# Kernel optimization log

Hardware: AMD Instinct MI355X
Metric: run time of the kernel (lower is better)

Reference implementation:

```python
import jax, jax.numpy as jnp
import numpy as np

B, S, H = 1, 2048, 2048
I = 1408
E = 64
TOP_K = 8
N_GROUP = 8
TOPK_GROUP = 4
SCALE = 2.5
N_SHARED = 2


def setup_inputs() -> dict:
    key = jax.random.key(0)
    ks = jax.random.split(key, 9)
    x = jax.random.normal(ks[0], (B, S, H), dtype=jnp.float32)
    # kaiming_uniform(a=sqrt(5)) for [E, H] weight -> bound = 1/sqrt(H)
    gate_w = jax.random.uniform(ks[1], (E, H), jnp.float32, -1.0, 1.0) / jnp.sqrt(float(H))
    e_bias = jnp.zeros((E,), jnp.float32)
    gate_proj = jax.random.normal(ks[2], (E, I, H), jnp.float32) * 0.02
    up_proj = jax.random.normal(ks[3], (E, I, H), jnp.float32) * 0.02
    down_proj = jax.random.normal(ks[4], (E, H, I), jnp.float32) * 0.02
    SI = I * N_SHARED
    shared_gate_w = jax.random.uniform(ks[5], (SI, H), jnp.float32, -1.0, 1.0) / jnp.sqrt(float(H))
    shared_up_w = jax.random.uniform(ks[6], (SI, H), jnp.float32, -1.0, 1.0) / jnp.sqrt(float(H))
    shared_down_w = jax.random.uniform(ks[7], (H, SI), jnp.float32, -1.0, 1.0) / jnp.sqrt(float(SI))
    return {"hidden_states": x, "gate_w": gate_w, "e_bias": e_bias,
            "gate_proj": gate_proj, "up_proj": up_proj, "down_proj": down_proj,
            "shared_gate_w": shared_gate_w, "shared_up_w": shared_up_w,
            "shared_down_w": shared_down_w}


def _moe_forward(hidden_states, gate_w, e_bias, gate_proj, up_proj, down_proj,
                 shared_gate_w, shared_up_w, shared_down_w):
    bsz, seq_len, h = hidden_states.shape
    xf = hidden_states.reshape(-1, h).astype(jnp.float32)  # [T, H]
    T = bsz * seq_len

    # ---- DeepSeek group-restricted top-k gating ----
    logits = xf @ gate_w.T                                  # [T, E]
    scores = jax.nn.sigmoid(logits)
    scores_for_choice = scores + e_bias[None, :]
    gs = scores_for_choice.reshape(T, N_GROUP, E // N_GROUP)
    group_scores = jax.lax.top_k(gs, 2)[0].sum(-1)          # [T, n_group] sum of top-2 per group
    group_idx = jax.lax.top_k(group_scores, TOPK_GROUP)[1]  # [T, topk_group]
    group_mask = jax.nn.one_hot(group_idx, N_GROUP, dtype=jnp.float32).sum(1)  # [T, n_group]
    score_mask = jnp.repeat(group_mask, E // N_GROUP, axis=1)                  # [T, E]
    tmp_scores = jnp.where(score_mask > 0, scores_for_choice, 0.0)
    topk_idx = jax.lax.top_k(tmp_scores, TOP_K)[1]          # [T, top_k]
    topk_w = jnp.take_along_axis(scores, topk_idx, axis=1)  # gather from UN-biased scores
    topk_w = topk_w / (topk_w.sum(-1, keepdims=True) + 1e-20)
    topk_w = topk_w * SCALE

    # Dense combine weights [T, E]; exactly equivalent to sort/dispatch/combine.
    rows = jnp.arange(T)
    cw = jnp.zeros((T, E), jnp.float32).at[rows[:, None], topk_idx].add(topk_w)

    # ---- per-expert FFN, accumulated with lax.scan over the (fixed) expert axis ----
    def step(y, we):
        Wg, Wu, Wd, w = we                                  # [I,H],[I,H],[H,I],[T]
        g = xf @ Wg.T                                       # [T, I]
        u = xf @ Wu.T
        inter = jax.nn.silu(g) * u                          # silu_mul kernel
        out = inter @ Wd.T                                  # [T, H]
        return y + out * w[:, None], None

    y0 = jnp.zeros_like(xf)
    y, _ = jax.lax.scan(step, y0, (gate_proj, up_proj, down_proj, cw.T))
    y = y.reshape(bsz, seq_len, h)

    # ---- shared experts ----
    sg = hidden_states @ shared_gate_w.T                    # [B, S, SI]
    su = hidden_states @ shared_up_w.T
    shared_out = (jax.nn.silu(sg) * su) @ shared_down_w.T   # [B, S, H]
    return y + shared_out


def reference(hidden_states, gate_w, e_bias, gate_proj, up_proj, down_proj,
              shared_gate_w, shared_up_w, shared_down_w):
    return _moe_forward(hidden_states, gate_w, e_bias, gate_proj, up_proj, down_proj,
                        shared_gate_w, shared_up_w, shared_down_w)
```

## Files before the change

kernel.cpp:

```cpp
#include <hip/hip_runtime.h>

typedef unsigned short u16;
typedef unsigned int u32;
typedef __attribute__((ext_vector_type(8))) short short8;
typedef __attribute__((ext_vector_type(8))) u16 ushort8;
typedef __attribute__((ext_vector_type(4))) float f32x4;

#define T_TOK 2048
#define H_DIM 2048
#define NEXP 64
#define I_DIM 1408
#define SI_DIM 2816
#define BM 128
#define BK 64
#define MAXT 384

__device__ __forceinline__ u16 f2bf(float f) {
    u32 u = __builtin_bit_cast(u32, f);
    u32 r = u + 0x7FFFu + ((u >> 16) & 1u);
    return (u16)(r >> 16);
}

__device__ __forceinline__ ushort8 cvt8(f32x4 a, f32x4 b) {
    ushort8 o;
    o[0] = f2bf(a[0]); o[1] = f2bf(a[1]); o[2] = f2bf(a[2]); o[3] = f2bf(a[3]);
    o[4] = f2bf(b[0]); o[5] = f2bf(b[1]); o[6] = f2bf(b[2]); o[7] = f2bf(b[3]);
    return o;
}

__device__ __forceinline__ f32x4 mfma16(short8 a, short8 b, f32x4 c) {
    return __builtin_amdgcn_mfma_f32_16x16x32_bf16(a, b, c, 0, 0, 0);
}

__global__ __launch_bounds__(256) void k_cvt(const float* __restrict__ x, u16* __restrict__ xb) {
    int i = (blockIdx.x * 256 + threadIdx.x) * 8;
    f32x4 v0 = *(const f32x4*)(x + i);
    f32x4 v1 = *(const f32x4*)(x + i + 4);
    *(ushort8*)(xb + i) = cvt8(v0, v1);
}

__global__ __launch_bounds__(256) void k_gate_logits(const float* __restrict__ x,
        const float* __restrict__ gw, float* __restrict__ logits) {
    __shared__ float xs[8][65];
    __shared__ float wsh[64][65];
    int tid = threadIdx.x;
    int t0 = blockIdx.x * 8;
    double acc0 = 0.0, acc1 = 0.0;
    int e = tid & 63, tg = tid >> 6;
    for (int k0 = 0; k0 < H_DIM; k0 += 64) {
        #pragma unroll
        for (int s = 0; s < 2; ++s) {
            int idx = s * 256 + tid;
            int r = idx >> 6, k = idx & 63;
            xs[r][k] = x[(size_t)(t0 + r) * H_DIM + k0 + k];
        }
        #pragma unroll
        for (int s = 0; s < 16; ++s) {
            int idx = s * 256 + tid;
            int r = idx >> 6, k = idx & 63;
            wsh[r][k] = gw[(size_t)r * H_DIM + k0 + k];
        }
        __syncthreads();
        #pragma unroll 8
        for (int k = 0; k < 64; ++k) {
            double wv = (double)wsh[e][k];
            acc0 += (double)xs[tg][k] * wv;
            acc1 += (double)xs[tg + 4][k] * wv;
        }
        __syncthreads();
    }
    logits[(size_t)(t0 + tg) * NEXP + e] = (float)acc0;
    logits[(size_t)(t0 + tg + 4) * NEXP + e] = (float)acc1;
}

__global__ __launch_bounds__(256) void k_topk(const float* __restrict__ logits,
        const float* __restrict__ ebias, int* __restrict__ topk_idx,
        float* __restrict__ topk_w, int* __restrict__ counts) {
    __shared__ float bsh[64];
    if (threadIdx.x < 64) bsh[threadIdx.x] = ebias[threadIdx.x];
    __syncthreads();
    int t = blockIdx.x * 256 + threadIdx.x;
    float sc[64];
    #pragma unroll
    for (int e2 = 0; e2 < 64; ++e2) {
        float lg = logits[(size_t)t * 64 + e2];
        sc[e2] = 1.0f / (1.0f + expf(-lg));
    }
    float gsc[8];
    #pragma unroll
    for (int g = 0; g < 8; ++g) {
        float m1 = -1e30f, m2 = -1e30f;
        #pragma unroll
        for (int j = 0; j < 8; ++j) {
            float v = sc[g * 8 + j] + bsh[g * 8 + j];
            if (v > m1) { m2 = m1; m1 = v; }
            else if (v > m2) { m2 = v; }
        }
        gsc[g] = m1 + m2;
    }
    u32 gmask = 0;
    #pragma unroll
    for (int it = 0; it < 4; ++it) {
        float best = -1e30f; int bi = 0;
        #pragma unroll
        for (int g = 0; g < 8; ++g) {
            bool ok = !((gmask >> g) & 1u);
            if (ok && gsc[g] > best) { best = gsc[g]; bi = g; }
        }
        gmask |= 1u << bi;
    }
    unsigned long long avail = 0ull;
    #pragma unroll
    for (int g = 0; g < 8; ++g)
        if ((gmask >> g) & 1u) avail |= (0xFFull << (g * 8));
    float wsum = 0.f;
    int idx[8]; float wv[8];
    #pragma unroll
    for (int it = 0; it < 8; ++it) {
        float best = -1e30f, bw = 0.f; int bi = 0;
        #pragma unroll
        for (int e2 = 0; e2 < 64; ++e2) {
            bool ok = (avail >> e2) & 1ull;
            float v = sc[e2] + bsh[e2];
            if (ok && v > best) { best = v; bi = e2; bw = sc[e2]; }
        }
        avail &= ~(1ull << bi);
        idx[it] = bi; wv[it] = bw; wsum += bw;
    }
    float scale = 2.5f / (wsum + 1e-20f);
    #pragma unroll
    for (int it = 0; it < 8; ++it) {
        topk_idx[t * 8 + it] = idx[it];
        topk_w[t * 8 + it] = wv[it] * scale;
        atomicAdd(&counts[idx[it]], 1);
    }
}

__global__ void k_prefix(const int* __restrict__ counts, int* __restrict__ offsets,
                         int* __restrict__ tiles, int* __restrict__ ntiles) {
    if (threadIdx.x == 0) {
        int run = 0;
        for (int e = 0; e < 64; ++e) { offsets[e] = run; run += counts[e]; }
        offsets[64] = run;
        for (int i = 0; i < MAXT; ++i) tiles[i] = -1;
        int slot[8] = {0, 0, 0, 0, 0, 0, 0, 0};
        int nt = 0;
        for (int e = 0; e < 64; ++e) {
            int xcd = e & 7;
            int c = counts[e];
            for (int m0 = 0; m0 < c; m0 += BM) {
                int pos = xcd + 8 * slot[xcd];
                if (pos < MAXT) { tiles[pos] = (e << 16) | m0; slot[xcd]++; nt++; }
            }
        }
        *ntiles = nt;
    }
}

__global__ __launch_bounds__(256) void k_scatter(const int* __restrict__ topk_idx,
        const float* __restrict__ topk_w, const int* __restrict__ offsets,
        int* __restrict__ fill, int* __restrict__ tok_list, float* __restrict__ w_list) {
    int gid = blockIdx.x * 256 + threadIdx.x;
    int t = gid >> 3;
    int e = topk_idx[gid];
    int pos = offsets[e] + atomicAdd(&fill[e], 1);
    tok_list[pos] = t;
    w_list[pos] = topk_w[gid];
}

__global__ __launch_bounds__(256, 2) void k_gateup(
        const u16* __restrict__ xb,
        const float* __restrict__ gate_base, const float* __restrict__ up_base,
        const int* __restrict__ offsets, const int* __restrict__ tok_list,
        const int* __restrict__ tiles, const int* __restrict__ ntiles,
        u16* __restrict__ inter, int Irows) {
    int e, m0, seg, n, i0;
    if (tiles) {
        int tt = tiles[blockIdx.x];
        if (tt < 0) return;
        e = tt >> 16; m0 = tt & 0xFFFF;
        seg = offsets[e]; n = offsets[e + 1] - seg;
        i0 = blockIdx.y * 64;
    } else {
        e = 0; seg = 0; n = T_TOK;
        i0 = blockIdx.x * 64;
        if (i0 >= Irows) return;
        m0 = blockIdx.y * BM;
    }
    if (n <= 0 || m0 >= n) return;

    const float* Bg = gate_base + (size_t)e * Irows * H_DIM;
    const float* Bu = up_base + (size_t)e * Irows * H_DIM;

    __shared__ u16 As[2][BM * BK];
    __shared__ u16 Bsg[2][64 * BK];
    __shared__ u16 Bsu[2][64 * BK];

    int tid = threadIdx.x;
    int w = tid >> 6, lane = tid & 63;

    const u16* asrc[4]; int adst[4];
    #pragma unroll
    for (int s = 0; s < 4; ++s) {
        int slot = s * 256 + tid;
        int r = slot >> 3, cb = slot & 7;
        int p = m0 + r; if (p >= n) p = n - 1;
        int tok = tok_list ? tok_list[seg + p] : p;
        asrc[s] = xb + (size_t)tok * H_DIM + cb * 8;
        adst[s] = r * BK + ((cb ^ (r & 7)) * 8);
    }
    const float* bgsrc[2]; const float* busrc[2]; int bdst[2];
    #pragma unroll
    for (int s = 0; s < 2; ++s) {
        int slot = s * 256 + tid;
        int r = slot >> 3, cb = slot & 7;
        bgsrc[s] = Bg + (size_t)(i0 + r) * H_DIM + cb * 8;
        busrc[s] = Bu + (size_t)(i0 + r) * H_DIM + cb * 8;
        bdst[s] = r * BK + ((cb ^ (r & 7)) * 8);
    }

    f32x4 zero; zero[0] = 0.f; zero[1] = 0.f; zero[2] = 0.f; zero[3] = 0.f;
    f32x4 accg[2][4], accu[2][4];
    #pragma unroll
    for (int a = 0; a < 2; ++a)
        #pragma unroll
        for (int b = 0; b < 4; ++b) { accg[a][b] = zero; accu[a][b] = zero; }

    short8 stA0[4], stA1[4];
    f32x4 stG0[2][2], stU0[2][2], stG1[2][2], stU1[2][2];

    auto ldS0 = [&](int t) {
        int k0 = t * BK;
        #pragma unroll
        for (int s = 0; s < 4; ++s) stA0[s] = *(const short8*)(asrc[s] + k0);
        #pragma unroll
        for (int s = 0; s < 2; ++s) {
            stG0[s][0] = *(const f32x4*)(bgsrc[s] + k0);
            stG0[s][1] = *(const f32x4*)(bgsrc[s] + k0 + 4);
            stU0[s][0] = *(const f32x4*)(busrc[s] + k0);
            stU0[s][1] = *(const f32x4*)(busrc[s] + k0 + 4);
        }
    };
    auto ldS1 = [&](int t) {
        int k0 = t * BK;
        #pragma unroll
        for (int s = 0; s < 4; ++s) stA1[s] = *(const short8*)(asrc[s] + k0);
        #pragma unroll
        for (int s = 0; s < 2; ++s) {
            stG1[s][0] = *(const f32x4*)(bgsrc[s] + k0);
            stG1[s][1] = *(const f32x4*)(bgsrc[s] + k0 + 4);
            stU1[s][0] = *(const f32x4*)(busrc[s] + k0);
            stU1[s][1] = *(const f32x4*)(busrc[s] + k0 + 4);
        }
    };
    auto dsw0 = [&]() {
        #pragma unroll
        for (int s = 0; s < 4; ++s) *(ushort8*)(&As[0][adst[s]]) = *(const ushort8*)&stA0[s];
        #pragma unroll
        for (int s = 0; s < 2; ++s) {
            *(ushort8*)(&Bsg[0][bdst[s]]) = cvt8(stG0[s][0], stG0[s][1]);
            *(ushort8*)(&Bsu[0][bdst[s]]) = cvt8(stU0[s][0], stU0[s][1]);
        }
    };
    auto dsw1 = [&]() {
        #pragma unroll
        for (int s = 0; s < 4; ++s) *(ushort8*)(&As[1][adst[s]]) = *(const ushort8*)&stA1[s];
        #pragma unroll
        for (int s = 0; s < 2; ++s) {
            *(ushort8*)(&Bsg[1][bdst[s]]) = cvt8(stG1[s][0], stG1[s][1]);
            *(ushort8*)(&Bsu[1][bdst[s]]) = cvt8(stU1[s][0], stU1[s][1]);
        }
    };
    auto mmaStep = [&](int buf) {
        #pragma unroll
        for (int ks = 0; ks < 2; ++ks) {
            short8 a[2];
            #pragma unroll
            for (int fm = 0; fm < 2; ++fm) {
                int row = w * 32 + fm * 16 + (lane & 15);
                int cb = ks * 4 + (lane >> 4);
                a[fm] = *(const short8*)(&As[buf][row * BK + ((cb ^ (row & 7)) * 8)]);
            }
            #pragma unroll
            for (int fn = 0; fn < 4; ++fn) {
                int brow = fn * 16 + (lane & 15);
                int cb = ks * 4 + (lane >> 4);
                int boff = brow * BK + ((cb ^ (brow & 7)) * 8);
                short8 bg = *(const short8*)(&Bsg[buf][boff]);
                short8 bu = *(const short8*)(&Bsu[buf][boff]);
                accg[0][fn] = mfma16(a[0], bg, accg[0][fn]);
                accg[1][fn] = mfma16(a[1], bg, accg[1][fn]);
                accu[0][fn] = mfma16(a[0], bu, accu[0][fn]);
                accu[1][fn] = mfma16(a[1], bu, accu[1][fn]);
            }
        }
    };

    const int NK = H_DIM / BK;
    ldS0(0); dsw0();
    ldS1(1);
    __syncthreads();
    for (int t = 0; t < NK; t += 2) {
        if (t + 2 < NK) ldS0(t + 2);
        mmaStep(0);
        if (t + 1 < NK) dsw1();
        __syncthreads();
        if (t + 1 < NK) {
            if (t + 3 < NK) ldS1(t + 3);
            mmaStep(1);
            if (t + 2 < NK) dsw0();
            __syncthreads();
        }
    }

    int r0 = (lane >> 4) * 4, cc = lane & 15;
    #pragma unroll
    for (int fm = 0; fm < 2; ++fm) {
        #pragma unroll
        for (int r = 0; r < 4; ++r) {
            int p = m0 + w * 32 + fm * 16 + r0 + r;
            if (p < n) {
                size_t rowb = (size_t)(seg + p) * Irows + i0;
                #pragma unroll
                for (int fn = 0; fn < 4; ++fn) {
                    float g = accg[fm][fn][r], u = accu[fm][fn][r];
                    float val = g / (1.0f + expf(-g)) * u;
                    inter[rowb + fn * 16 + cc] = f2bf(val);
                }
            }
        }
    }
}

__global__ __launch_bounds__(256, 2) void k_down(
        const u16* __restrict__ inter, int Kdim,
        const float* __restrict__ down_base,
        const int* __restrict__ offsets, const int* __restrict__ tok_list,
        const int* __restrict__ tiles, const int* __restrict__ ntiles,
        const float* __restrict__ w_list,
        float* __restrict__ out) {
    int e, m0, seg, n, h0;
    if (tiles) {
        int tt = tiles[blockIdx.x];
        if (tt < 0) return;
        e = tt >> 16; m0 = tt & 0xFFFF;
        seg = offsets[e]; n = offsets[e + 1] - seg;
        h0 = blockIdx.y * 128;
    } else {
        e = 0; seg = 0; n = T_TOK;
        h0 = blockIdx.x * 128;
        m0 = blockIdx.y * BM;
    }
    if (n <= 0 || m0 >= n) return;

    const float* Bd = down_base + (size_t)e * H_DIM * Kdim;

    __shared__ u16 As[2][BM * BK];
    __shared__ u16 Bs[2][128 * BK];

    int tid = threadIdx.x;
    int w = tid >> 6, lane = tid & 63;

    const u16* asrc[4]; int adst[4];
    #pragma unroll
    for (int s = 0; s < 4; ++s) {
        int slot = s * 256 + tid;
        int r = slot >> 3, cb = slot & 7;
        int p = m0 + r; if (p >= n) p = n - 1;
        asrc[s] = inter + (size_t)(seg + p) * Kdim + cb * 8;
        adst[s] = r * BK + ((cb ^ (r & 7)) * 8);
    }
    const float* bsrc[4]; int bdst[4];
    #pragma unroll
    for (int s = 0; s < 4; ++s) {
        int slot = s * 256 + tid;
        int r = slot >> 3, cb = slot & 7;
        bsrc[s] = Bd + (size_t)(h0 + r) * Kdim + cb * 8;
        bdst[s] = r * BK + ((cb ^ (r & 7)) * 8);
    }

    f32x4 zero; zero[0] = 0.f; zero[1] = 0.f; zero[2] = 0.f; zero[3] = 0.f;
    f32x4 acc[2][8];
    #pragma unroll
    for (int a = 0; a < 2; ++a)
        #pragma unroll
        for (int b = 0; b < 8; ++b) acc[a][b] = zero;

    short8 stA0[4], stA1[4];
    f32x4 stB0[4][2], stB1[4][2];

    auto ldS0 = [&](int t) {
        int k0 = t * BK;
        #pragma unroll
        for (int s = 0; s < 4; ++s) stA0[s] = *(const short8*)(asrc[s] + k0);
        #pragma unroll
        for (int s = 0; s < 4; ++s) {
            stB0[s][0] = *(const f32x4*)(bsrc[s] + k0);
            stB0[s][1] = *(const f32x4*)(bsrc[s] + k0 + 4);
        }
    };
    auto ldS1 = [&](int t) {
        int k0 = t * BK;
        #pragma unroll
        for (int s = 0; s < 4; ++s) stA1[s] = *(const short8*)(asrc[s] + k0);
        #pragma unroll
        for (int s = 0; s < 4; ++s) {
            stB1[s][0] = *(const f32x4*)(bsrc[s] + k0);
            stB1[s][1] = *(const f32x4*)(bsrc[s] + k0 + 4);
        }
    };
    auto dsw0 = [&]() {
        #pragma unroll
        for (int s = 0; s < 4; ++s) *(ushort8*)(&As[0][adst[s]]) = *(const ushort8*)&stA0[s];
        #pragma unroll
        for (int s = 0; s < 4; ++s)
            *(ushort8*)(&Bs[0][bdst[s]]) = cvt8(stB0[s][0], stB0[s][1]);
    };
    auto dsw1 = [&]() {
        #pragma unroll
        for (int s = 0; s < 4; ++s) *(ushort8*)(&As[1][adst[s]]) = *(const ushort8*)&stA1[s];
        #pragma unroll
        for (int s = 0; s < 4; ++s)
            *(ushort8*)(&Bs[1][bdst[s]]) = cvt8(stB1[s][0], stB1[s][1]);
    };
    auto mmaStep = [&](int buf) {
        #pragma unroll
        for (int ks = 0; ks < 2; ++ks) {
            short8 a[2];
            #pragma unroll
            for (int fm = 0; fm < 2; ++fm) {
                int row = w * 32 + fm * 16 + (lane & 15);
                int cb = ks * 4 + (lane >> 4);
                a[fm] = *(const short8*)(&As[buf][row * BK + ((cb ^ (row & 7)) * 8)]);
            }
            #pragma unroll
            for (int fn = 0; fn < 8; ++fn) {
                int brow = fn * 16 + (lane & 15);
                int cb = ks * 4 + (lane >> 4);
                short8 b = *(const short8*)(&Bs[buf][brow * BK + ((cb ^ (brow & 7)) * 8)]);
                acc[0][fn] = mfma16(a[0], b, acc[0][fn]);
                acc[1][fn] = mfma16(a[1], b, acc[1][fn]);
            }
        }
    };

    const int NK = Kdim / BK;
    ldS0(0); dsw0();
    ldS1(1);
    __syncthreads();
    for (int t = 0; t < NK; t += 2) {
        if (t + 2 < NK) ldS0(t + 2);
        mmaStep(0);
        if (t + 1 < NK) dsw1();
        __syncthreads();
        if (t + 1 < NK) {
            if (t + 3 < NK) ldS1(t + 3);
            mmaStep(1);
            if (t + 2 < NK) dsw0();
            __syncthreads();
        }
    }

    int r0 = (lane >> 4) * 4, cc = lane & 15;
    #pragma unroll
    for (int fm = 0; fm < 2; ++fm) {
        #pragma unroll
        for (int r = 0; r < 4; ++r) {
            int p = m0 + w * 32 + fm * 16 + r0 + r;
            if (p < n) {
                int tok = tok_list ? tok_list[seg + p] : p;
                size_t ob = (size_t)tok * H_DIM + h0 + cc;
                if (w_list) {
                    float wt = w_list[seg + p];
                    #pragma unroll
                    for (int fn = 0; fn < 8; ++fn)
                        atomicAdd(&out[ob + fn * 16], acc[fm][fn][r] * wt);
                } else {
                    #pragma unroll
                    for (int fn = 0; fn < 8; ++fn)
                        out[ob + fn * 16] = acc[fm][fn][r];
                }
            }
        }
    }
}

extern "C" void kernel_launch(void* const* d_in, const int* in_sizes, int n_in,
                              void* d_out, int out_size, void* d_ws, size_t ws_size,
                              hipStream_t stream) {
    const float* x         = (const float*)d_in[0];
    const float* gate_w    = (const float*)d_in[1];
    const float* e_bias    = (const float*)d_in[2];
    const float* gate_proj = (const float*)d_in[3];
    const float* up_proj   = (const float*)d_in[4];
    const float* down_proj = (const float*)d_in[5];
    const float* sgw       = (const float*)d_in[6];
    const float* suw       = (const float*)d_in[7];
    const float* sdw       = (const float*)d_in[8];
    float* out = (float*)d_out;

    char* ws = (char*)d_ws;
    size_t off = 0;
    auto alloc = [&](size_t bytes) -> char* {
        char* p = ws + off;
        off += (bytes + 255) & ~(size_t)255;
        return p;
    };
    float* logits   = (float*)alloc((size_t)T_TOK * 64 * 4);
    int*   topk_idx = (int*)  alloc((size_t)T_TOK * 8 * 4);
    float* topk_w   = (float*)alloc((size_t)T_TOK * 8 * 4);
    int*   counts   = (int*)  alloc(256);
    int*   offsets  = (int*)  alloc(512);
    int*   fill     = (int*)  alloc(256);
    int*   tiles    = (int*)  alloc(MAXT * 4);
    int*   ntiles   = (int*)  alloc(256);
    int*   tok_list = (int*)  alloc((size_t)T_TOK * 8 * 4);
    float* w_list   = (float*)alloc((size_t)T_TOK * 8 * 4);
    u16*   xb       = (u16*)  alloc((size_t)T_TOK * H_DIM * 2);
    u16*   inter    = (u16*)  alloc((size_t)T_TOK * 8 * I_DIM * 2);

    hipMemsetAsync(counts, 0, 1024, stream);

    k_cvt<<<(T_TOK * H_DIM) / 2048, 256, 0, stream>>>(x, xb);
    k_gate_logits<<<T_TOK / 8, 256, 0, stream>>>(x, gate_w, logits);
    k_topk<<<T_TOK / 256, 256, 0, stream>>>(logits, e_bias, topk_idx, topk_w, counts);
    k_prefix<<<1, 64, 0, stream>>>(counts, offsets, tiles, ntiles);
    k_scatter<<<(T_TOK * 8) / 256, 256, 0, stream>>>(topk_idx, topk_w, offsets, fill, tok_list, w_list);

    k_gateup<<<dim3(48, T_TOK / BM), 256, 0, stream>>>(
        xb, sgw, suw, nullptr, nullptr, nullptr, nullptr, inter, SI_DIM);
    k_down<<<dim3(16, T_TOK / BM), 256, 0, stream>>>(
        inter, SI_DIM, sdw, nullptr, nullptr, nullptr, nullptr, nullptr, out);

    k_gateup<<<dim3(MAXT, I_DIM / 64), 256, 0, stream>>>(
        xb, gate_proj, up_proj, offsets, tok_list, tiles, ntiles, inter, I_DIM);
    k_down<<<dim3(MAXT, H_DIM / 128), 256, 0, stream>>>(
        inter, I_DIM, down_proj, offsets, tok_list, tiles, ntiles, w_list, out);
}
```

Measured before the change: 1.301 ms.

## Merge shared-expert GEMMs into routed grouped GEMM launches via unified tile list

Shared-expert gate/up and down GEMMs are encoded as extra tiles (expert id 64) in per-kernel tile lists, so a single gate/up launch and a single down launch cover both shared and routed work. This removes two launches and the tail idle time between the dependent shared and routed GEMM phases. In exchange the output must be zeroed by a memset, shared outputs use atomics instead of plain stores, MAXT grows and more idle blocks are launched, and a separate buffer holds the shared intermediate.

After: 1.331 ms. 1.02x slower.

```diff
diff --git a/kernel.cpp b/kernel.cpp
--- a/kernel.cpp
+++ b/kernel.cpp
@@ -13,7 +13,7 @@
 #define SI_DIM 2816
 #define BM 128
 #define BK 64
-#define MAXT 384
+#define MAXT 512
 
 __device__ __forceinline__ u16 f2bf(float f) {
     u32 u = __builtin_bit_cast(u32, f);
@@ -137,23 +137,34 @@
 }
 
 __global__ void k_prefix(const int* __restrict__ counts, int* __restrict__ offsets,
-                         int* __restrict__ tiles, int* __restrict__ ntiles) {
+                         int* __restrict__ tiles_gu, int* __restrict__ tiles_dn) {
     if (threadIdx.x == 0) {
         int run = 0;
         for (int e = 0; e < 64; ++e) { offsets[e] = run; run += counts[e]; }
         offsets[64] = run;
-        for (int i = 0; i < MAXT; ++i) tiles[i] = -1;
-        int slot[8] = {0, 0, 0, 0, 0, 0, 0, 0};
-        int nt = 0;
+        for (int i = 0; i < MAXT; ++i) { tiles_gu[i] = -1; tiles_dn[i] = -1; }
+        int sg[8] = {0,0,0,0,0,0,0,0};
+        int sd[8] = {0,0,0,0,0,0,0,0};
+        for (int j = 0; j < SI_DIM / 64; ++j) {
+            int xcd = j & 7;
+            int pos = xcd + 8 * sg[xcd];
+            if (pos < MAXT) { tiles_gu[pos] = (64 << 16) | (j * 64); sg[xcd]++; }
+        }
+        for (int j = 0; j < H_DIM / 128; ++j) {
+            int xcd = j & 7;
+            int pos = xcd + 8 * sd[xcd];
+            if (pos < MAXT) { tiles_dn[pos] = (64 << 16) | (j * 128); sd[xcd]++; }
+        }
         for (int e = 0; e < 64; ++e) {
             int xcd = e & 7;
             int c = counts[e];
             for (int m0 = 0; m0 < c; m0 += BM) {
-                int pos = xcd + 8 * slot[xcd];
-                if (pos < MAXT) { tiles[pos] = (e << 16) | m0; slot[xcd]++; nt++; }
-            }
-        }
-        *ntiles = nt;
+                int pg = xcd + 8 * sg[xcd];
+                if (pg < MAXT) { tiles_gu[pg] = (e << 16) | m0; sg[xcd]++; }
+                int pd = xcd + 8 * sd[xcd];
+                if (pd < MAXT) { tiles_dn[pd] = (e << 16) | m0; sd[xcd]++; }
+            }
+        }
     }
 }
 
@@ -170,27 +181,29 @@
 
 __global__ __launch_bounds__(256, 2) void k_gateup(
         const u16* __restrict__ xb,
-        const float* __restrict__ gate_base, const float* __restrict__ up_base,
+        const float* __restrict__ gr, const float* __restrict__ ur,
+        const float* __restrict__ gs, const float* __restrict__ us,
         const int* __restrict__ offsets, const int* __restrict__ tok_list,
-        const int* __restrict__ tiles, const int* __restrict__ ntiles,
-        u16* __restrict__ inter, int Irows) {
-    int e, m0, seg, n, i0;
-    if (tiles) {
-        int tt = tiles[blockIdx.x];
-        if (tt < 0) return;
-        e = tt >> 16; m0 = tt & 0xFFFF;
-        seg = offsets[e]; n = offsets[e + 1] - seg;
+        const int* __restrict__ tiles,
+        u16* __restrict__ inter_r, u16* __restrict__ inter_s) {
+    int tt = tiles[blockIdx.x];
+    if (tt < 0) return;
+    int e = tt >> 16;
+    const float *Bg, *Bu; u16* op; const int* tl;
+    int m0, seg, n, i0, Irows;
+    if (e < 64) {
+        m0 = tt & 0xFFFF; seg = offsets[e]; n = offsets[e + 1] - seg;
+        if (n <= 0 || m0 >= n) return;
         i0 = blockIdx.y * 64;
+        Bg = gr + (size_t)e * I_DIM * H_DIM;
+        Bu = ur + (size_t)e * I_DIM * H_DIM;
+        op = inter_r; Irows = I_DIM; tl = tok_list;
     } else {
-        e = 0; seg = 0; n = T_TOK;
-        i0 = blockIdx.x * 64;
-        if (i0 >= Irows) return;
-        m0 = blockIdx.y * BM;
-    }
-    if (n <= 0 || m0 >= n) return;
-
-    const float* Bg = gate_base + (size_t)e * Irows * H_DIM;
-    const float* Bu = up_base + (size_t)e * Irows * H_DIM;
+        if (blockIdx.y >= T_TOK / BM) return;
+        i0 = tt & 0xFFFF; m0 = blockIdx.y * BM; seg = 0; n = T_TOK;
+        Bg = gs; Bu = us;
+        op = inter_s; Irows = SI_DIM; tl = nullptr;
+    }
 
     __shared__ u16 As[2][BM * BK];
     __shared__ u16 Bsg[2][64 * BK];
@@ -205,7 +218,7 @@
         int slot = s * 256 + tid;
         int r = slot >> 3, cb = slot & 7;
         int p = m0 + r; if (p >= n) p = n - 1;
-        int tok = tok_list ? tok_list[seg + p] : p;
+        int tok = tl ? tl[seg + p] : p;
         asrc[s] = xb + (size_t)tok * H_DIM + cb * 8;
         adst[s] = r * BK + ((cb ^ (r & 7)) * 8);
     }
@@ -325,7 +338,7 @@
                 for (int fn = 0; fn < 4; ++fn) {
                     float g = accg[fm][fn][r], u = accu[fm][fn][r];
                     float val = g / (1.0f + expf(-g)) * u;
-                    inter[rowb + fn * 16 + cc] = f2bf(val);
+                    op[rowb + fn * 16 + cc] = f2bf(val);
                 }
             }
         }
@@ -333,27 +346,27 @@
 }
 
 __global__ __launch_bounds__(256, 2) void k_down(
-        const u16* __restrict__ inter, int Kdim,
-        const float* __restrict__ down_base,
+        const u16* __restrict__ inter_r, const u16* __restrict__ inter_s,
+        const float* __restrict__ dr, const float* __restrict__ dsw,
         const int* __restrict__ offsets, const int* __restrict__ tok_list,
-        const int* __restrict__ tiles, const int* __restrict__ ntiles,
+        const int* __restrict__ tiles,
         const float* __restrict__ w_list,
         float* __restrict__ out) {
-    int e, m0, seg, n, h0;
-    if (tiles) {
-        int tt = tiles[blockIdx.x];
-        if (tt < 0) return;
-        e = tt >> 16; m0 = tt & 0xFFFF;
-        seg = offsets[e]; n = offsets[e + 1] - seg;
+    int tt = tiles[blockIdx.x];
+    if (tt < 0) return;
+    int e = tt >> 16;
+    const float* Bd; const u16* interp; const int* tl; const float* wl;
+    int m0, seg, n, h0, Kdim;
+    if (e < 64) {
+        m0 = tt & 0xFFFF; seg = offsets[e]; n = offsets[e + 1] - seg;
+        if (n <= 0 || m0 >= n) return;
         h0 = blockIdx.y * 128;
+        Bd = dr + (size_t)e * H_DIM * I_DIM;
+        interp = inter_r; Kdim = I_DIM; tl = tok_list; wl = w_list;
     } else {
-        e = 0; seg = 0; n = T_TOK;
-        h0 = blockIdx.x * 128;
-        m0 = blockIdx.y * BM;
-    }
-    if (n <= 0 || m0 >= n) return;
-
-    const float* Bd = down_base + (size_t)e * H_DIM * Kdim;
+        h0 = tt & 0xFFFF; m0 = blockIdx.y * BM; seg = 0; n = T_TOK;
+        Bd = dsw; interp = inter_s; Kdim = SI_DIM; tl = nullptr; wl = nullptr;
+    }
 
     __shared__ u16 As[2][BM * BK];
     __shared__ u16 Bs[2][128 * BK];
@@ -367,7 +380,7 @@
         int slot = s * 256 + tid;
         int r = slot >> 3, cb = slot & 7;
         int p = m0 + r; if (p >= n) p = n - 1;
-        asrc[s] = inter + (size_t)(seg + p) * Kdim + cb * 8;
+        asrc[s] = interp + (size_t)(seg + p) * Kdim + cb * 8;
         adst[s] = r * BK + ((cb ^ (r & 7)) * 8);
     }
     const float* bsrc[4]; int bdst[4];
@@ -468,18 +481,12 @@
         for (int r = 0; r < 4; ++r) {
             int p = m0 + w * 32 + fm * 16 + r0 + r;
             if (p < n) {
-                int tok = tok_list ? tok_list[seg + p] : p;
+                int tok = tl ? tl[seg + p] : p;
+                float wt = wl ? wl[seg + p] : 1.0f;
                 size_t ob = (size_t)tok * H_DIM + h0 + cc;
-                if (w_list) {
-                    float wt = w_list[seg + p];
-                    #pragma unroll
-                    for (int fn = 0; fn < 8; ++fn)
-                        atomicAdd(&out[ob + fn * 16], acc[fm][fn][r] * wt);
-                } else {
-                    #pragma unroll
-                    for (int fn = 0; fn < 8; ++fn)
-                        out[ob + fn * 16] = acc[fm][fn][r];
-                }
+                #pragma unroll
+                for (int fn = 0; fn < 8; ++fn)
+                    atomicAdd(&out[ob + fn * 16], acc[fm][fn][r] * wt);
             }
         }
     }
@@ -512,28 +519,27 @@
     int*   counts   = (int*)  alloc(256);
     int*   offsets  = (int*)  alloc(512);
     int*   fill     = (int*)  alloc(256);
-    int*   tiles    = (int*)  alloc(MAXT * 4);
-    int*   ntiles   = (int*)  alloc(256);
+    int*   tiles_gu = (int*)  alloc(MAXT * 4);
+    int*   tiles_dn = (int*)  alloc(MAXT * 4);
     int*   tok_list = (int*)  alloc((size_t)T_TOK * 8 * 4);
     float* w_list   = (float*)alloc((size_t)T_TOK * 8 * 4);
     u16*   xb       = (u16*)  alloc((size_t)T_TOK * H_DIM * 2);
-    u16*   inter    = (u16*)  alloc((size_t)T_TOK * 8 * I_DIM * 2);
+    u16*   inter_r  = (u16*)  alloc((size_t)T_TOK * 8 * I_DIM * 2);
+    u16*   inter_s  = (u16*)  alloc((size_t)T_TOK * SI_DIM * 2);
 
     hipMemsetAsync(counts, 0, 1024, stream);
+    hipMemsetAsync(out, 0, (size_t)out_size * 4, stream);
 
     k_cvt<<<(T_TOK * H_DIM) / 2048, 256, 0, stream>>>(x, xb);
     k_gate_logits<<<T_TOK / 8, 256, 0, stream>>>(x, gate_w, logits);
     k_topk<<<T_TOK / 256, 256, 0, stream>>>(logits, e_bias, topk_idx, topk_w, counts);
-    k_prefix<<<1, 64, 0, stream>>>(counts, offsets, tiles, ntiles);
+    k_prefix<<<1, 64, 0, stream>>>(counts, offsets, tiles_gu, tiles_dn);
     k_scatter<<<(T_TOK * 8) / 256, 256, 0, stream>>>(topk_idx, topk_w, offsets, fill, tok_list, w_list);
 
-    k_gateup<<<dim3(48, T_TOK / BM), 256, 0, stream>>>(
-        xb, sgw, suw, nullptr, nullptr, nullptr, nullptr, inter, SI_DIM);
-    k_down<<<dim3(16, T_TOK / BM), 256, 0, stream>>>(
-        inter, SI_DIM, sdw, nullptr, nullptr, nullptr, nullptr, nullptr, out);
-
     k_gateup<<<dim3(MAXT, I_DIM / 64), 256, 0, stream>>>(
-        xb, gate_proj, up_proj, offsets, tok_list, tiles, ntiles, inter, I_DIM);
+        xb, gate_proj, up_proj, sgw, suw, offsets, tok_list, tiles_gu,
+        inter_r, inter_s);
     k_down<<<dim3(MAXT, H_DIM / 128), 256, 0, stream>>>(
-        inter, I_DIM, down_proj, offsets, tok_list, tiles, ntiles, w_list, out);
-}
+        inter_r, inter_s, down_proj, sdw, offsets, tok_list, tiles_dn,
+        w_list, out);
+}
```
